# Optimization experiments

Measured on AMD Instinct MI355X. Metric: run time of the kernel, lower is better.

Reference implementation:

```python
import jax, jax.numpy as jnp
import numpy as np
from jax import lax

B, N, C, RED = 8, 2048, 1024, 4
GN_EPS = 1e-5


def setup_inputs() -> dict:
    key = jax.random.key(0)
    ks = jax.random.split(key, 8)
    s = lambda k, shp, sc: jax.random.normal(k, shp, jnp.float32) * sc
    return dict(
        x=jax.random.normal(ks[0], (B, N, C), jnp.float32),
        qkv_w=s(ks[1], (C, 3 * C), 0.02),
        c1=jnp.float32(0.01 ** 2),
        c2=jnp.float32(0.03 ** 2),
        conv1_w=s(ks[2], (4, 1, 3), 0.3),      # OIH
        gn_g=jnp.ones(4, jnp.float32),
        gn_b=jnp.zeros(4, jnp.float32),
        conv2_w=s(ks[3], (1, 4, 3), 0.3),      # OIH
        conv2_b=jnp.zeros(1, jnp.float32),
        ch_w1=s(ks[4], (C, C // RED), 0.02),
        ch_b1=jnp.zeros(C // RED, jnp.float32),
        ch_w2=s(ks[5], (C // RED, C), 0.02),
        ch_b2=jnp.zeros(C, jnp.float32),
        proj_w=s(ks[6], (C, C), 0.02),
        proj_b=jnp.zeros(C, jnp.float32),
    )


def _conv1d(x, w):  # x:[B,Cin,N], w:[O,I,3], pad=1
    return lax.conv_general_dilated(x, w, (1,), [(1, 1)],
                                    dimension_numbers=('NCH', 'OIH', 'NCH'))


def _ode_func(A, conv1_w, gn_g, gn_b, conv2_w, conv2_b):
    # A: [B,N] -> Conv1d(1,4) -> GroupNorm(2,4) -> ReLU -> Conv1d(4,1)
    h = _conv1d(A[:, None, :], conv1_w)                 # [B,4,N]
    b, _, n = h.shape
    hg = h.reshape(b, 2, 2, n)                          # 2 groups of 2 channels
    mu = hg.mean((2, 3), keepdims=True)
    var = hg.var((2, 3), keepdims=True)
    h = ((hg - mu) * lax.rsqrt(var + GN_EPS)).reshape(b, 4, n)
    h = jax.nn.relu(h * gn_g[None, :, None] + gn_b[None, :, None])
    y = _conv1d(h, conv2_w) + conv2_b[None, :, None]    # [B,1,N]
    return y[:, 0, :]


def reference(x, qkv_w, c1, c2, conv1_w, gn_g, gn_b, conv2_w, conv2_b,
              ch_w1, ch_b1, ch_w2, ch_b2, proj_w, proj_b):
    Bx, Nx, Cx = x.shape
    qkv = (x @ qkv_w).reshape(Bx, Nx, 3, Cx)
    q, k, v = qkv[..., 0, :], qkv[..., 1, :], qkv[..., 2, :]

    # SSIM-style per-token statistics over the channel dim
    mu_q = q.mean(-1, keepdims=True)
    mu_k = k.mean(-1, keepdims=True)
    dq, dk = q - mu_q, k - mu_k
    inv_cm1 = 1.0 / (Cx - 1)
    sigma_qk = (dq * dk).sum(-1, keepdims=True) * inv_cm1
    sigma_q2 = (dq * dq).sum(-1, keepdims=True) * inv_cm1
    sigma_k2 = (dk * dk).sum(-1, keepdims=True) * inv_cm1
    num = (2 * mu_q * mu_k + c1) * (2 * sigma_qk + c2)
    den = (mu_q ** 2 + mu_k ** 2 + c1) * (sigma_q2 + sigma_k2 + c2)
    attn_base = ((num / (den + 1e-7)) ** 2)[..., 0]     # [B,N]

    # explicit-Euler integration over t = linspace(0,1,2) -> one step, dt=1
    steps = 2
    ts = jnp.linspace(0.0, 1.0, steps)
    dts = ts[1:] - ts[:-1]

    def step(A, dt):
        return A + dt * _ode_func(A, conv1_w, gn_g, gn_b, conv2_w, conv2_b), None

    A, _ = lax.scan(step, attn_base, dts)
    final_a = jax.nn.sigmoid(A)                         # [B,N]
    weights = jax.nn.softmax(final_a, axis=1)           # softmax over tokens

    # channel gating from mean token
    m = x.mean(axis=1, keepdims=True)                   # [B,1,C]
    ch_w = jax.nn.sigmoid(jax.nn.relu(m @ ch_w1 + ch_b1) @ ch_w2 + ch_b2)

    out_low = weights[..., None] * v * ch_w             # [B,N,C]
    return out_low @ proj_w + proj_b
```

## Files before the change

kernel.cpp:

```cpp
#include <hip/hip_runtime.h>

typedef __attribute__((ext_vector_type(8))) short short8;
typedef __attribute__((ext_vector_type(4))) short short4v;
typedef __attribute__((ext_vector_type(4))) float floatx4;

__device__ __forceinline__ unsigned short f2bf(float f) {
    unsigned u = __float_as_uint(f);
    u = u + 0x7fffu + ((u >> 16) & 1u);
    return (unsigned short)(u >> 16);
}

__device__ __forceinline__ void gl_lds16(const void* g, void* l) {
    __builtin_amdgcn_global_load_lds((const __attribute__((address_space(1))) void*)g,
                                     (__attribute__((address_space(3))) void*)l, 16, 0, 0);
}

__global__ __launch_bounds__(256) void convmean_kernel(const float* __restrict__ x,
                                                       short* __restrict__ xb,
                                                       float* __restrict__ part) {
    int bid = blockIdx.x;
    int b = bid >> 6, nch = bid & 63;
    int tid = threadIdx.x;
    size_t base = ((size_t)b * 2048 + nch * 32) * 1024;
    float s0 = 0.f, s1 = 0.f, s2 = 0.f, s3 = 0.f;
    int c0 = tid * 4;
    for (int r = 0; r < 32; r++) {
        const float* rp = x + base + (size_t)r * 1024 + c0;
        float4 v = *(const float4*)rp;
        s0 += v.x; s1 += v.y; s2 += v.z; s3 += v.w;
        short4v o;
        o[0] = (short)f2bf(v.x); o[1] = (short)f2bf(v.y);
        o[2] = (short)f2bf(v.z); o[3] = (short)f2bf(v.w);
        *(short4v*)(xb + base + (size_t)r * 1024 + c0) = o;
    }
    float* pp = part + ((size_t)b * 64 + nch) * 1024 + c0;
    float4 ps; ps.x = s0; ps.y = s1; ps.z = s2; ps.w = s3;
    *(float4*)pp = ps;
}

__global__ __launch_bounds__(256) void transpose_conv_kernel(const float* __restrict__ w_qkv,
                                                             short* __restrict__ qkvT,
                                                             const float* __restrict__ w_proj,
                                                             short* __restrict__ projT) {
    __shared__ float t[64][65];
    int bx = blockIdx.x;
    const float* in; short* out; int C; bool is_qkv;
    int c0, r0 = blockIdx.y * 64;
    if (bx < 48) { in = w_qkv; out = qkvT; C = 3072; c0 = bx * 64; is_qkv = true; }
    else         { in = w_proj; out = projT; C = 1024; c0 = (bx - 48) * 64; is_qkv = false; }
    int tid = threadIdx.x;
#pragma unroll
    for (int l = 0; l < 16; l++) {
        int idx = l * 256 + tid;
        int rr = idx >> 6, cc = idx & 63;
        t[rr][cc] = in[(size_t)(r0 + rr) * C + c0 + cc];
    }
    __syncthreads();
#pragma unroll
    for (int l = 0; l < 16; l++) {
        int idx = l * 256 + tid;
        int rr = idx >> 6, cc = idx & 63;
        int ro = c0 + rr;
        int rnew = ro;
        if (is_qkv) {
            if (ro < 1024) rnew = 2 * ro;
            else if (ro < 2048) rnew = 2 * (ro - 1024) + 1;
        }
        out[(size_t)rnew * 1024 + r0 + cc] = (short)f2bf(t[cc][rr]);
    }
}

__global__ __launch_bounds__(256) void ch_kernel(const float* __restrict__ part,
                                                 const float* __restrict__ w1,
                                                 const float* __restrict__ b1,
                                                 const float* __restrict__ w2,
                                                 const float* __restrict__ b2,
                                                 float* __restrict__ ch) {
    int b = blockIdx.x >> 3, cg = blockIdx.x & 7;
    int tid = threadIdx.x;
    __shared__ float mrow[1024];
    __shared__ float hid[256];
    for (int i = tid; i < 1024; i += 256) {
        float s = 0.f;
        for (int j = 0; j < 64; j++) s += part[((size_t)b * 64 + j) * 1024 + i];
        mrow[i] = s * (1.f / 2048.f);
    }
    __syncthreads();
    {
        float s0 = 0.f, s1 = 0.f, s2 = 0.f, s3 = 0.f;
        for (int i = 0; i < 1024; i += 4) {
            s0 += mrow[i] * w1[(size_t)i * 256 + tid];
            s1 += mrow[i + 1] * w1[(size_t)(i + 1) * 256 + tid];
            s2 += mrow[i + 2] * w1[(size_t)(i + 2) * 256 + tid];
            s3 += mrow[i + 3] * w1[(size_t)(i + 3) * 256 + tid];
        }
        hid[tid] = fmaxf((s0 + s1) + (s2 + s3) + b1[tid], 0.f);
    }
    __syncthreads();
    if (tid < 128) {
        int c = cg * 128 + tid;
        float s0 = 0.f, s1 = 0.f, s2 = 0.f, s3 = 0.f;
        for (int j = 0; j < 256; j += 4) {
            s0 += hid[j] * w2[(size_t)j * 1024 + c];
            s1 += hid[j + 1] * w2[(size_t)(j + 1) * 1024 + c];
            s2 += hid[j + 2] * w2[(size_t)(j + 2) * 1024 + c];
            s3 += hid[j + 3] * w2[(size_t)(j + 3) * 1024 + c];
        }
        float s = (s0 + s1) + (s2 + s3) + b2[c];
        ch[(size_t)b * 1024 + c] = 1.f / (1.f + expf(-s));
    }
}


#define QKV_PHASE(qq)                                                                   \
    {                                                                                   \
        _Pragma("unroll")                                                               \
        for (int ii = 0; ii < 4; ii++)                                                  \
            af[ii] = *(const short8*)(As_ + (wm * 128 + ((qq)*4 + ii) * 16 + ar) * 32 + swq); \
        __builtin_amdgcn_s_setprio(1);                                                  \
        _Pragma("unroll")                                                               \
        for (int ii = 0; ii < 4; ii++)                                                  \
            _Pragma("unroll")                                                           \
            for (int jj = 0; jj < 4; jj++)                                              \
                acc[(qq)*4 + ii][jj] =                                                  \
                    __builtin_amdgcn_mfma_f32_16x16x32_bf16(af[ii], bfr[jj], acc[(qq)*4 + ii][jj], 0, 0, 0); \
        __builtin_amdgcn_s_setprio(0);                                                  \
    }

#define LOAD_B()                                                                        \
    {                                                                                   \
        _Pragma("unroll")                                                               \
        for (int jj = 0; jj < 4; jj++)                                                  \
            bfr[jj] = *(const short8*)(Bs_ + (wn * 64 + jj * 16 + ar) * 32 + swq);      \
    }

__global__ __launch_bounds__(512, 2) void gemm_qkv_kernel(const short* __restrict__ A,
                                                          const short* __restrict__ BT,
                                                          short* __restrict__ vbuf,
                                                          const float* __restrict__ ch,
                                                          float* __restrict__ part2)
{
    __shared__ __align__(16) short ASf[4 * 8192];
    __shared__ __align__(16) short BSf[4 * 8192];
    const int tid = threadIdx.x;
    const int wave = tid >> 6, lane = tid & 63;
    const int id = blockIdx.x;
    const int xcd = id & 7, j = id >> 3;
    const int bn = j % 12;
    const int bmg = j / 12;
    const int bm = bmg * 8 + xcd;
    const int wm = wave >> 2, wn = wave & 3;
    const int ar = lane & 15, quad = lane >> 4;
    const int swq = (quad ^ ((ar >> 1) & 3)) * 8;

    const int swzk = ((lane & 3) ^ ((lane >> 3) & 3)) * 8;
    const short* Ag = A + (size_t)(bm * 256 + wave * 32 + (lane >> 2)) * 1024 + swzk;
    const short* Bg = BT + (size_t)(bn * 256 + wave * 32 + (lane >> 2)) * 1024 + swzk;
    short* ASw = ASf + wave * 1024;
    short* BSw = BSf + wave * 1024;

    floatx4 acc[8][4];
    floatx4 zero = {0.f, 0.f, 0.f, 0.f};
#pragma unroll
    for (int i = 0; i < 8; i++)
#pragma unroll
        for (int jj = 0; jj < 4; jj++) acc[i][jj] = zero;

    auto stageA = [&](int t) {
        const int sl = (t & 3) * 8192, ko = t * 32;
        gl_lds16(Ag + ko, ASw + sl);
        gl_lds16(Ag + (size_t)16 * 1024 + ko, ASw + sl + 512);
    };
    auto stageB = [&](int t) {
        const int sl = (t & 3) * 8192, ko = t * 32;
        gl_lds16(Bg + ko, BSw + sl);
        gl_lds16(Bg + (size_t)16 * 1024 + ko, BSw + sl + 512);
    };

    short8 af[4], bfr[4];

    stageA(0); stageB(0); stageA(1); stageB(1);
    for (int t = 0; t < 30; ++t) {
        stageA(t + 2);
        asm volatile("s_waitcnt vmcnt(6)" ::: "memory");
        asm volatile("s_barrier" ::: "memory");
        const short* As_ = ASf + (t & 3) * 8192;
        const short* Bs_ = BSf + (t & 3) * 8192;
        LOAD_B();
        QKV_PHASE(0);
        stageB(t + 2);
        QKV_PHASE(1);
    }
    {
        asm volatile("s_waitcnt vmcnt(4)" ::: "memory");
        asm volatile("s_barrier" ::: "memory");
        const short* As_ = ASf + (30 & 3) * 8192;
        const short* Bs_ = BSf + (30 & 3) * 8192;
        LOAD_B();
        QKV_PHASE(0);
        QKV_PHASE(1);
    }
    {
        asm volatile("s_waitcnt vmcnt(0)" ::: "memory");
        asm volatile("s_barrier" ::: "memory");
        const short* As_ = ASf + (31 & 3) * 8192;
        const short* Bs_ = BSf + (31 & 3) * 8192;
        LOAD_B();
        QKV_PHASE(0);
        QKV_PHASE(1);
    }
    __syncthreads();

    if (bn < 8) {
        float* sb = (float*)ASf;
#pragma unroll
        for (int i = 0; i < 8; i++) {
            float st[4][5];
#pragma unroll
            for (int r = 0; r < 4; r++)
#pragma unroll
                for (int f = 0; f < 5; f++) st[r][f] = 0.f;
#pragma unroll
            for (int jj = 0; jj < 4; jj++) {
#pragma unroll
                for (int r = 0; r < 4; r++) {
                    float val = acc[i][jj][r];
                    float other = __shfl_xor(val, 1);
                    float q = (lane & 1) ? other : val;
                    float kv = (lane & 1) ? val : other;
                    st[r][0] += q; st[r][1] += kv;
                    st[r][2] += q * q; st[r][3] += kv * kv; st[r][4] += q * kv;
                }
            }
#pragma unroll
            for (int r = 0; r < 4; r++)
#pragma unroll
                for (int f = 0; f < 5; f++) {
                    float v = st[r][f];
                    v += __shfl_xor(v, 2);
                    v += __shfl_xor(v, 4);
                    v += __shfl_xor(v, 8);
                    st[r][f] = v;
                }
            if ((lane & 15) == 0) {
#pragma unroll
                for (int r = 0; r < 4; r++)
#pragma unroll
                    for (int f = 0; f < 5; f++)
                        sb[(size_t)(wn * 256 + wm * 128 + i * 16 + quad * 4 + r) * 5 + f] = st[r][f];
            }
        }
        __syncthreads();
        if (tid < 256) {
#pragma unroll
            for (int f = 0; f < 5; f++) {
                float s = sb[(size_t)(0 * 256 + tid) * 5 + f] + sb[(size_t)(1 * 256 + tid) * 5 + f] +
                          sb[(size_t)(2 * 256 + tid) * 5 + f] + sb[(size_t)(3 * 256 + tid) * 5 + f];
                part2[(size_t)(bn * 5 + f) * 16384 + bm * 256 + tid] = s;
            }
        }
    } else {
        const int batch = bm >> 3;
        const int vcol0 = bn * 256 - 2048 + wn * 64;
        short* pbuf = (short*)ASf + wave * 1024;
        float cw[4];
#pragma unroll
        for (int jj = 0; jj < 4; jj++) cw[jj] = ch[(size_t)batch * 1024 + vcol0 + jj * 16 + ar];
#pragma unroll
        for (int i = 0; i < 8; i++) {
#pragma unroll
            for (int jj = 0; jj < 4; jj++)
#pragma unroll
                for (int r = 0; r < 4; r++)
                    pbuf[(quad * 4 + r) * 64 + jj * 16 + ar] = (short)f2bf(acc[i][jj][r] * cw[jj]);
#pragma unroll
            for (int p = 0; p < 2; p++) {
                int idx = p * 512 + lane * 8;
                short8 vv = *(const short8*)(pbuf + idx);
                int grow = bm * 256 + wm * 128 + i * 16 + (idx >> 6);
                int gcol = vcol0 + (idx & 63);
                *(short8*)(vbuf + (size_t)grow * 1024 + gcol) = vv;
            }
        }
    }
}

__global__ __launch_bounds__(256) void finalize_kernel(const float* __restrict__ part2,
                                                       const float* __restrict__ c1p,
                                                       const float* __restrict__ c2p,
                                                       float* __restrict__ attn) {
    int row = blockIdx.x * 256 + threadIdx.x;
    float s[5] = {0.f, 0.f, 0.f, 0.f, 0.f};
#pragma unroll
    for (int slot = 0; slot < 8; slot++)
#pragma unroll
        for (int f = 0; f < 5; f++)
            s[f] += part2[(size_t)((slot * 5 + f) << 14) + row];
    const float C = 1024.f, invcm1 = 1.f / 1023.f;
    float c1 = *c1p, c2 = *c2p;
    float muq = s[0] / C, muk = s[1] / C;
    float sigqk = (s[4] - C * muq * muk) * invcm1;
    float sigq2 = (s[2] - C * muq * muq) * invcm1;
    float sigk2 = (s[3] - C * muk * muk) * invcm1;
    float num = (2.f * muq * muk + c1) * (2.f * sigqk + c2);
    float den = (muq * muq + muk * muk + c1) * (sigq2 + sigk2 + c2);
    float r = num / (den + 1e-7f);
    attn[row] = r * r;
}

__device__ __forceinline__ float blk_sum(float v, float* buf) {
#pragma unroll
    for (int m = 1; m < 64; m <<= 1) v += __shfl_xor(v, m);
    int wave = threadIdx.x >> 6;
    if ((threadIdx.x & 63) == 0) buf[wave] = v;
    __syncthreads();
    float r = buf[0] + buf[1] + buf[2] + buf[3];
    __syncthreads();
    return r;
}
__device__ __forceinline__ float blk_max(float v, float* buf) {
#pragma unroll
    for (int m = 1; m < 64; m <<= 1) v = fmaxf(v, __shfl_xor(v, m));
    int wave = threadIdx.x >> 6;
    if ((threadIdx.x & 63) == 0) buf[wave] = v;
    __syncthreads();
    float r = fmaxf(fmaxf(buf[0], buf[1]), fmaxf(buf[2], buf[3]));
    __syncthreads();
    return r;
}

__global__ __launch_bounds__(256) void ode_softmax_kernel(const float* __restrict__ attn,
                                                          const float* __restrict__ w1,
                                                          const float* __restrict__ gng,
                                                          const float* __restrict__ gnb,
                                                          const float* __restrict__ w2,
                                                          const float* __restrict__ b2,
                                                          float* __restrict__ wgt) {
    int b = blockIdx.x, tid = threadIdx.x;
    __shared__ float A0[2048];
    __shared__ float H[4][2048];
    __shared__ float rbuf[4];
    for (int i = tid; i < 2048; i += 256) A0[i] = attn[(size_t)b * 2048 + i];
    __syncthreads();
    float w1l[12], w2l[12];
#pragma unroll
    for (int i = 0; i < 12; i++) { w1l[i] = w1[i]; w2l[i] = w2[i]; }
    float gg[4], gb[4];
#pragma unroll
    for (int c = 0; c < 4; c++) { gg[c] = gng[c]; gb[c] = gnb[c]; }

    float s0 = 0.f, ss0 = 0.f, s1 = 0.f, ss1 = 0.f;
    for (int i = tid; i < 2048; i += 256) {
        float le = (i > 0) ? A0[i - 1] : 0.f;
        float mi = A0[i];
        float ri = (i < 2047) ? A0[i + 1] : 0.f;
#pragma unroll
        for (int c = 0; c < 4; c++) {
            float h = w1l[c * 3] * le + w1l[c * 3 + 1] * mi + w1l[c * 3 + 2] * ri;
            H[c][i] = h;
            if (c < 2) { s0 += h; ss0 += h * h; } else { s1 += h; ss1 += h * h; }
        }
    }
    s0 = blk_sum(s0, rbuf);
    ss0 = blk_sum(ss0, rbuf);
    s1 = blk_sum(s1, rbuf);
    ss1 = blk_sum(ss1, rbuf);
    float mu0 = s0 / 4096.f, var0 = ss0 / 4096.f - mu0 * mu0;
    float mu1 = s1 / 4096.f, var1 = ss1 / 4096.f - mu1 * mu1;
    float is0 = 1.f / sqrtf(var0 + 1e-5f);
    float is1 = 1.f / sqrtf(var1 + 1e-5f);

    for (int i = tid; i < 2048; i += 256) {
#pragma unroll
        for (int c = 0; c < 4; c++) {
            float inv = (c < 2) ? is0 : is1;
            float mu = (c < 2) ? mu0 : mu1;
            float v = (H[c][i] - mu) * inv * gg[c] + gb[c];
            H[c][i] = fmaxf(v, 0.f);
        }
    }
    __syncthreads();

    float bias2 = b2[0];
    float myfa[8];
    float lmax = -1e30f;
#pragma unroll
    for (int ii = 0; ii < 8; ii++) {
        int i = tid + ii * 256;
        float y = bias2;
#pragma unroll
        for (int c = 0; c < 4; c++) {
            float le = (i > 0) ? H[c][i - 1] : 0.f;
            float mi = H[c][i];
            float ri = (i < 2047) ? H[c][i + 1] : 0.f;
            y += w2l[c * 3] * le + w2l[c * 3 + 1] * mi + w2l[c * 3 + 2] * ri;
        }
        float Av = A0[i] + y;
        float fa = 1.f / (1.f + expf(-Av));
        myfa[ii] = fa;
        lmax = fmaxf(lmax, fa);
    }
    float gmax = blk_max(lmax, rbuf);
    float lsum = 0.f;
#pragma unroll
    for (int ii = 0; ii < 8; ii++) {
        myfa[ii] = expf(myfa[ii] - gmax);
        lsum += myfa[ii];
    }
    float gsum = blk_sum(lsum, rbuf);
    float inv = 1.f / gsum;
#pragma unroll
    for (int ii = 0; ii < 8; ii++) wgt[(size_t)b * 2048 + tid + ii * 256] = myfa[ii] * inv;
}

__global__ __launch_bounds__(512, 2) void gemm_out_kernel(const short* __restrict__ vbuf,
                                                          const short* __restrict__ BT,
                                                          const float* __restrict__ wgt,
                                                          const float* __restrict__ pb,
                                                          float* __restrict__ Out)
{
    __shared__ __align__(16) short ASf[4 * 8192];
    __shared__ __align__(16) short BSf[4 * 8192];
    const int tid = threadIdx.x;
    const int wave = tid >> 6, lane = tid & 63;
    const int id = blockIdx.x;
    const int xcd = id & 7, j = id >> 3;
    const int bn = j & 3;
    const int bmg = j >> 2;
    const int bm = bmg * 8 + xcd;
    const int wm = wave >> 2, wn = wave & 3;
    const int ar = lane & 15, quad = lane >> 4;
    const int swq = (quad ^ ((ar >> 1) & 3)) * 8;

    const int swzk = ((lane & 3) ^ ((lane >> 3) & 3)) * 8;
    const short* Ag = vbuf + (size_t)(bm * 256 + wave * 32 + (lane >> 2)) * 1024 + swzk;
    const short* Bg = BT + (size_t)(bn * 256 + wave * 32 + (lane >> 2)) * 1024 + swzk;
    short* ASw = ASf + wave * 1024;
    short* BSw = BSf + wave * 1024;

    floatx4 acc[8][4];
    floatx4 zero = {0.f, 0.f, 0.f, 0.f};
#pragma unroll
    for (int i = 0; i < 8; i++)
#pragma unroll
        for (int jj = 0; jj < 4; jj++) acc[i][jj] = zero;

    auto stageA = [&](int t) {
        const int sl = (t & 3) * 8192, ko = t * 32;
        gl_lds16(Ag + ko, ASw + sl);
        gl_lds16(Ag + (size_t)16 * 1024 + ko, ASw + sl + 512);
    };
    auto stageB = [&](int t) {
        const int sl = (t & 3) * 8192, ko = t * 32;
        gl_lds16(Bg + ko, BSw + sl);
        gl_lds16(Bg + (size_t)16 * 1024 + ko, BSw + sl + 512);
    };

    short8 af[4], bfr[4];

    stageA(0); stageB(0); stageA(1); stageB(1);
    for (int t = 0; t < 30; ++t) {
        stageA(t + 2);
        asm volatile("s_waitcnt vmcnt(6)" ::: "memory");
        asm volatile("s_barrier" ::: "memory");
        const short* As_ = ASf + (t & 3) * 8192;
        const short* Bs_ = BSf + (t & 3) * 8192;
        LOAD_B();
        QKV_PHASE(0);
        stageB(t + 2);
        QKV_PHASE(1);
    }
    {
        asm volatile("s_waitcnt vmcnt(4)" ::: "memory");
        asm volatile("s_barrier" ::: "memory");
        const short* As_ = ASf + (30 & 3) * 8192;
        const short* Bs_ = BSf + (30 & 3) * 8192;
        LOAD_B();
        QKV_PHASE(0);
        QKV_PHASE(1);
    }
    {
        asm volatile("s_waitcnt vmcnt(0)" ::: "memory");
        asm volatile("s_barrier" ::: "memory");
        const short* As_ = ASf + (31 & 3) * 8192;
        const short* Bs_ = BSf + (31 & 3) * 8192;
        LOAD_B();
        QKV_PHASE(0);
        QKV_PHASE(1);
    }
    __syncthreads();

    const int row0 = bm * 256 + wm * 128;
    const int col0 = bn * 256 + wn * 64;
    float* obuf = (float*)ASf + wave * 1024;
#pragma unroll
    for (int i = 0; i < 8; i++) {
#pragma unroll
        for (int jj = 0; jj < 4; jj++) {
            float bias = pb[col0 + jj * 16 + ar];
#pragma unroll
            for (int r = 0; r < 4; r++) {
                int grow = row0 + i * 16 + quad * 4 + r;
                obuf[(quad * 4 + r) * 64 + jj * 16 + ar] = wgt[grow] * acc[i][jj][r] + bias;
            }
        }
#pragma unroll
        for (int p = 0; p < 4; p++) {
            int idx = p * 256 + lane * 4;
            float4 vv = *(const float4*)(obuf + idx);
            int grow = row0 + i * 16 + (idx >> 6);
            int gcol = col0 + (idx & 63);
            *(float4*)(Out + (size_t)grow * 1024 + gcol) = vv;
        }
    }
}

extern "C" void kernel_launch(void* const* d_in, const int* in_sizes, int n_in,
                              void* d_out, int out_size, void* d_ws, size_t ws_size,
                              hipStream_t stream) {
    const float* x       = (const float*)d_in[0];
    const float* qkv_w   = (const float*)d_in[1];
    const float* c1      = (const float*)d_in[2];
    const float* c2      = (const float*)d_in[3];
    const float* conv1_w = (const float*)d_in[4];
    const float* gn_g    = (const float*)d_in[5];
    const float* gn_b    = (const float*)d_in[6];
    const float* conv2_w = (const float*)d_in[7];
    const float* conv2_b = (const float*)d_in[8];
    const float* ch_w1   = (const float*)d_in[9];
    const float* ch_b1   = (const float*)d_in[10];
    const float* ch_w2   = (const float*)d_in[11];
    const float* ch_b2   = (const float*)d_in[12];
    const float* proj_w  = (const float*)d_in[13];
    const float* proj_b  = (const float*)d_in[14];
    float* out = (float*)d_out;

    size_t off = 0;
    char* base = (char*)d_ws;
    auto carve = [&](size_t bytes) -> char* {
        char* p = base + off;
        off += (bytes + 255) & ~(size_t)255;
        return p;
    };
    short* x_bf  = (short*)carve((size_t)16384 * 1024 * 2);
    short* qkvT  = (short*)carve((size_t)3072 * 1024 * 2);
    short* projT = (short*)carve((size_t)1024 * 1024 * 2);
    short* vbuf  = (short*)carve((size_t)16384 * 1024 * 2);
    float* part2 = (float*)carve((size_t)80 * 16384 * 4);
    float* attn  = (float*)carve((size_t)16384 * 4);
    float* wgt   = (float*)carve((size_t)16384 * 4);
    float* part  = (float*)carve((size_t)8 * 64 * 1024 * 4);
    float* chw   = (float*)carve((size_t)8 * 1024 * 4);

    convmean_kernel<<<512, 256, 0, stream>>>(x, x_bf, part);
    transpose_conv_kernel<<<dim3(64, 16), 256, 0, stream>>>(qkv_w, qkvT, proj_w, projT);
    ch_kernel<<<64, 256, 0, stream>>>(part, ch_w1, ch_b1, ch_w2, ch_b2, chw);
    gemm_qkv_kernel<<<768, 512, 0, stream>>>(x_bf, qkvT, vbuf, chw, part2);
    finalize_kernel<<<64, 256, 0, stream>>>(part2, c1, c2, attn);
    ode_softmax_kernel<<<8, 256, 0, stream>>>(attn, conv1_w, gn_g, gn_b, conv2_w, conv2_b, wgt);
    gemm_out_kernel<<<256, 512, 0, stream>>>(vbuf, projT, wgt, proj_b, out);
}
```

Baseline: 390.9 us.

## Deepen GEMM prefetch to three stages, merge prep kernels, widen ODE softmax block

Both GEMM kernels now prefetch three k-tiles ahead instead of two, using the 4-slot LDS ring with vmcnt(8). The aim is to hide more global-load latency behind MFMA work. The x conversion/mean kernel and the weight transpose kernel are merged into one launch, which removes a launch and lets the two run concurrently. The ODE/softmax kernel moves from 256 to 1024 threads per block to add parallelism, at the cost of 16-wave reductions.

```diff
diff --git a/kernel.cpp b/kernel.cpp
--- a/kernel.cpp
+++ b/kernel.cpp
@@ -15,58 +15,59 @@
                                      (__attribute__((address_space(3))) void*)l, 16, 0, 0);
 }
 
-__global__ __launch_bounds__(256) void convmean_kernel(const float* __restrict__ x,
-                                                       short* __restrict__ xb,
-                                                       float* __restrict__ part) {
-    int bid = blockIdx.x;
-    int b = bid >> 6, nch = bid & 63;
+__global__ __launch_bounds__(256) void prep_kernel(const float* __restrict__ x,
+                                                   short* __restrict__ xb,
+                                                   float* __restrict__ part,
+                                                   const float* __restrict__ w_qkv,
+                                                   short* __restrict__ qkvT,
+                                                   const float* __restrict__ w_proj,
+                                                   short* __restrict__ projT) {
+    __shared__ float t[64][65];
     int tid = threadIdx.x;
-    size_t base = ((size_t)b * 2048 + nch * 32) * 1024;
-    float s0 = 0.f, s1 = 0.f, s2 = 0.f, s3 = 0.f;
-    int c0 = tid * 4;
-    for (int r = 0; r < 32; r++) {
-        const float* rp = x + base + (size_t)r * 1024 + c0;
-        float4 v = *(const float4*)rp;
-        s0 += v.x; s1 += v.y; s2 += v.z; s3 += v.w;
-        short4v o;
-        o[0] = (short)f2bf(v.x); o[1] = (short)f2bf(v.y);
-        o[2] = (short)f2bf(v.z); o[3] = (short)f2bf(v.w);
-        *(short4v*)(xb + base + (size_t)r * 1024 + c0) = o;
-    }
-    float* pp = part + ((size_t)b * 64 + nch) * 1024 + c0;
-    float4 ps; ps.x = s0; ps.y = s1; ps.z = s2; ps.w = s3;
-    *(float4*)pp = ps;
-}
-
-__global__ __launch_bounds__(256) void transpose_conv_kernel(const float* __restrict__ w_qkv,
-                                                             short* __restrict__ qkvT,
-                                                             const float* __restrict__ w_proj,
-                                                             short* __restrict__ projT) {
-    __shared__ float t[64][65];
-    int bx = blockIdx.x;
-    const float* in; short* out; int C; bool is_qkv;
-    int c0, r0 = blockIdx.y * 64;
-    if (bx < 48) { in = w_qkv; out = qkvT; C = 3072; c0 = bx * 64; is_qkv = true; }
-    else         { in = w_proj; out = projT; C = 1024; c0 = (bx - 48) * 64; is_qkv = false; }
-    int tid = threadIdx.x;
-#pragma unroll
-    for (int l = 0; l < 16; l++) {
-        int idx = l * 256 + tid;
-        int rr = idx >> 6, cc = idx & 63;
-        t[rr][cc] = in[(size_t)(r0 + rr) * C + c0 + cc];
-    }
-    __syncthreads();
-#pragma unroll
-    for (int l = 0; l < 16; l++) {
-        int idx = l * 256 + tid;
-        int rr = idx >> 6, cc = idx & 63;
-        int ro = c0 + rr;
-        int rnew = ro;
-        if (is_qkv) {
-            if (ro < 1024) rnew = 2 * ro;
-            else if (ro < 2048) rnew = 2 * (ro - 1024) + 1;
-        }
-        out[(size_t)rnew * 1024 + r0 + cc] = (short)f2bf(t[cc][rr]);
+    if (blockIdx.x < 512) {
+        int bid = blockIdx.x;
+        int b = bid >> 6, nch = bid & 63;
+        size_t base = ((size_t)b * 2048 + nch * 32) * 1024;
+        float s0 = 0.f, s1 = 0.f, s2 = 0.f, s3 = 0.f;
+        int c0 = tid * 4;
+        for (int r = 0; r < 32; r++) {
+            const float* rp = x + base + (size_t)r * 1024 + c0;
+            float4 v = *(const float4*)rp;
+            s0 += v.x; s1 += v.y; s2 += v.z; s3 += v.w;
+            short4v o;
+            o[0] = (short)f2bf(v.x); o[1] = (short)f2bf(v.y);
+            o[2] = (short)f2bf(v.z); o[3] = (short)f2bf(v.w);
+            *(short4v*)(xb + base + (size_t)r * 1024 + c0) = o;
+        }
+        float* pp = part + ((size_t)b * 64 + nch) * 1024 + c0;
+        float4 ps; ps.x = s0; ps.y = s1; ps.z = s2; ps.w = s3;
+        *(float4*)pp = ps;
+    } else {
+        int mb = blockIdx.x - 512;
+        int bx = mb & 63, by = mb >> 6;
+        const float* in; short* out; int C; bool is_qkv;
+        int c0, r0 = by * 64;
+        if (bx < 48) { in = w_qkv; out = qkvT; C = 3072; c0 = bx * 64; is_qkv = true; }
+        else         { in = w_proj; out = projT; C = 1024; c0 = (bx - 48) * 64; is_qkv = false; }
+#pragma unroll
+        for (int l = 0; l < 16; l++) {
+            int idx = l * 256 + tid;
+            int rr = idx >> 6, cc = idx & 63;
+            t[rr][cc] = in[(size_t)(r0 + rr) * C + c0 + cc];
+        }
+        __syncthreads();
+#pragma unroll
+        for (int l = 0; l < 16; l++) {
+            int idx = l * 256 + tid;
+            int rr = idx >> 6, cc = idx & 63;
+            int ro = c0 + rr;
+            int rnew = ro;
+            if (is_qkv) {
+                if (ro < 1024) rnew = 2 * ro;
+                else if (ro < 2048) rnew = 2 * (ro - 1024) + 1;
+            }
+            out[(size_t)rnew * 1024 + r0 + cc] = (short)f2bf(t[cc][rr]);
+        }
     }
 }
 
@@ -179,16 +180,25 @@
 
     short8 af[4], bfr[4];
 
-    stageA(0); stageB(0); stageA(1); stageB(1);
-    for (int t = 0; t < 30; ++t) {
-        stageA(t + 2);
-        asm volatile("s_waitcnt vmcnt(6)" ::: "memory");
+    stageA(0); stageB(0); stageA(1); stageB(1); stageA(2); stageB(2);
+    for (int t = 0; t < 29; ++t) {
+        asm volatile("s_waitcnt vmcnt(8)" ::: "memory");
         asm volatile("s_barrier" ::: "memory");
         const short* As_ = ASf + (t & 3) * 8192;
         const short* Bs_ = BSf + (t & 3) * 8192;
         LOAD_B();
-        QKV_PHASE(0);
-        stageB(t + 2);
+        stageA(t + 3);
+        QKV_PHASE(0);
+        stageB(t + 3);
+        QKV_PHASE(1);
+    }
+    {
+        asm volatile("s_waitcnt vmcnt(8)" ::: "memory");
+        asm volatile("s_barrier" ::: "memory");
+        const short* As_ = ASf + (29 & 3) * 8192;
+        const short* Bs_ = BSf + (29 & 3) * 8192;
+        LOAD_B();
+        QKV_PHASE(0);
         QKV_PHASE(1);
     }
     {
@@ -308,39 +318,43 @@
     attn[row] = r * r;
 }
 
-__device__ __forceinline__ float blk_sum(float v, float* buf) {
+__device__ __forceinline__ float blk_sum16(float v, float* buf) {
 #pragma unroll
     for (int m = 1; m < 64; m <<= 1) v += __shfl_xor(v, m);
     int wave = threadIdx.x >> 6;
     if ((threadIdx.x & 63) == 0) buf[wave] = v;
     __syncthreads();
-    float r = buf[0] + buf[1] + buf[2] + buf[3];
+    float r = 0.f;
+#pragma unroll
+    for (int w = 0; w < 16; w++) r += buf[w];
     __syncthreads();
     return r;
 }
-__device__ __forceinline__ float blk_max(float v, float* buf) {
+__device__ __forceinline__ float blk_max16(float v, float* buf) {
 #pragma unroll
     for (int m = 1; m < 64; m <<= 1) v = fmaxf(v, __shfl_xor(v, m));
     int wave = threadIdx.x >> 6;
     if ((threadIdx.x & 63) == 0) buf[wave] = v;
     __syncthreads();
-    float r = fmaxf(fmaxf(buf[0], buf[1]), fmaxf(buf[2], buf[3]));
+    float r = -1e30f;
+#pragma unroll
+    for (int w = 0; w < 16; w++) r = fmaxf(r, buf[w]);
     __syncthreads();
     return r;
 }
 
-__global__ __launch_bounds__(256) void ode_softmax_kernel(const float* __restrict__ attn,
-                                                          const float* __restrict__ w1,
-                                                          const float* __restrict__ gng,
-                                                          const float* __restrict__ gnb,
-                                                          const float* __restrict__ w2,
-                                                          const float* __restrict__ b2,
-                                                          float* __restrict__ wgt) {
+__global__ __launch_bounds__(1024) void ode_softmax_kernel(const float* __restrict__ attn,
+                                                           const float* __restrict__ w1,
+                                                           const float* __restrict__ gng,
+                                                           const float* __restrict__ gnb,
+                                                           const float* __restrict__ w2,
+                                                           const float* __restrict__ b2,
+                                                           float* __restrict__ wgt) {
     int b = blockIdx.x, tid = threadIdx.x;
     __shared__ float A0[2048];
     __shared__ float H[4][2048];
-    __shared__ float rbuf[4];
-    for (int i = tid; i < 2048; i += 256) A0[i] = attn[(size_t)b * 2048 + i];
+    __shared__ float rbuf[16];
+    for (int i = tid; i < 2048; i += 1024) A0[i] = attn[(size_t)b * 2048 + i];
     __syncthreads();
     float w1l[12], w2l[12];
 #pragma unroll
@@ -350,7 +364,7 @@
     for (int c = 0; c < 4; c++) { gg[c] = gng[c]; gb[c] = gnb[c]; }
 
     float s0 = 0.f, ss0 = 0.f, s1 = 0.f, ss1 = 0.f;
-    for (int i = tid; i < 2048; i += 256) {
+    for (int i = tid; i < 2048; i += 1024) {
         float le = (i > 0) ? A0[i - 1] : 0.f;
         float mi = A0[i];
         float ri = (i < 2047) ? A0[i + 1] : 0.f;
@@ -361,16 +375,16 @@
             if (c < 2) { s0 += h; ss0 += h * h; } else { s1 += h; ss1 += h * h; }
         }
     }
-    s0 = blk_sum(s0, rbuf);
-    ss0 = blk_sum(ss0, rbuf);
-    s1 = blk_sum(s1, rbuf);
-    ss1 = blk_sum(ss1, rbuf);
+    s0 = blk_sum16(s0, rbuf);
+    ss0 = blk_sum16(ss0, rbuf);
+    s1 = blk_sum16(s1, rbuf);
+    ss1 = blk_sum16(ss1, rbuf);
     float mu0 = s0 / 4096.f, var0 = ss0 / 4096.f - mu0 * mu0;
     float mu1 = s1 / 4096.f, var1 = ss1 / 4096.f - mu1 * mu1;
     float is0 = 1.f / sqrtf(var0 + 1e-5f);
     float is1 = 1.f / sqrtf(var1 + 1e-5f);
 
-    for (int i = tid; i < 2048; i += 256) {
+    for (int i = tid; i < 2048; i += 1024) {
 #pragma unroll
         for (int c = 0; c < 4; c++) {
             float inv = (c < 2) ? is0 : is1;
@@ -382,11 +396,11 @@
     __syncthreads();
 
     float bias2 = b2[0];
-    float myfa[8];
+    float myfa[2];
     float lmax = -1e30f;
 #pragma unroll
-    for (int ii = 0; ii < 8; ii++) {
-        int i = tid + ii * 256;
+    for (int ii = 0; ii < 2; ii++) {
+        int i = tid + ii * 1024;
         float y = bias2;
 #pragma unroll
         for (int c = 0; c < 4; c++) {
@@ -400,17 +414,17 @@
         myfa[ii] = fa;
         lmax = fmaxf(lmax, fa);
     }
-    float gmax = blk_max(lmax, rbuf);
+    float gmax = blk_max16(lmax, rbuf);
     float lsum = 0.f;
 #pragma unroll
-    for (int ii = 0; ii < 8; ii++) {
+    for (int ii = 0; ii < 2; ii++) {
         myfa[ii] = expf(myfa[ii] - gmax);
         lsum += myfa[ii];
     }
-    float gsum = blk_sum(lsum, rbuf);
+    float gsum = blk_sum16(lsum, rbuf);
     float inv = 1.f / gsum;
 #pragma unroll
-    for (int ii = 0; ii < 8; ii++) wgt[(size_t)b * 2048 + tid + ii * 256] = myfa[ii] * inv;
+    for (int ii = 0; ii < 2; ii++) wgt[(size_t)b * 2048 + tid + ii * 1024] = myfa[ii] * inv;
 }
 
 __global__ __launch_bounds__(512, 2) void gemm_out_kernel(const short* __restrict__ vbuf,
@@ -458,16 +472,25 @@
 
     short8 af[4], bfr[4];
 
-    stageA(0); stageB(0); stageA(1); stageB(1);
-    for (int t = 0; t < 30; ++t) {
-        stageA(t + 2);
-        asm volatile("s_waitcnt vmcnt(6)" ::: "memory");
+    stageA(0); stageB(0); stageA(1); stageB(1); stageA(2); stageB(2);
+    for (int t = 0; t < 29; ++t) {
+        asm volatile("s_waitcnt vmcnt(8)" ::: "memory");
         asm volatile("s_barrier" ::: "memory");
         const short* As_ = ASf + (t & 3) * 8192;
         const short* Bs_ = BSf + (t & 3) * 8192;
         LOAD_B();
-        QKV_PHASE(0);
-        stageB(t + 2);
+        stageA(t + 3);
+        QKV_PHASE(0);
+        stageB(t + 3);
+        QKV_PHASE(1);
+    }
+    {
+        asm volatile("s_waitcnt vmcnt(8)" ::: "memory");
+        asm volatile("s_barrier" ::: "memory");
+        const short* As_ = ASf + (29 & 3) * 8192;
+        const short* Bs_ = BSf + (29 & 3) * 8192;
+        LOAD_B();
+        QKV_PHASE(0);
         QKV_PHASE(1);
     }
     {
@@ -552,11 +575,10 @@
     float* part  = (float*)carve((size_t)8 * 64 * 1024 * 4);
     float* chw   = (float*)carve((size_t)8 * 1024 * 4);
 
-    convmean_kernel<<<512, 256, 0, stream>>>(x, x_bf, part);
-    transpose_conv_kernel<<<dim3(64, 16), 256, 0, stream>>>(qkv_w, qkvT, proj_w, projT);
+    prep_kernel<<<1536, 256, 0, stream>>>(x, x_bf, part, qkv_w, qkvT, proj_w, projT);
     ch_kernel<<<64, 256, 0, stream>>>(part, ch_w1, ch_b1, ch_w2, ch_b2, chw);
     gemm_qkv_kernel<<<768, 512, 0, stream>>>(x_bf, qkvT, vbuf, chw, part2);
     finalize_kernel<<<64, 256, 0, stream>>>(part2, c1, c2, attn);
-    ode_softmax_kernel<<<8, 256, 0, stream>>>(attn, conv1_w, gn_g, gn_b, conv2_w, conv2_b, wgt);
+    ode_softmax_kernel<<<8, 1024, 0, stream>>>(attn, conv1_w, gn_g, gn_b, conv2_w, conv2_b, wgt);
     gemm_out_kernel<<<256, 512, 0, stream>>>(vbuf, projT, wgt, proj_b, out);
 }
```

New measurement: 411.6 us. 1.05x slower.
